# Optimization experiments

Hardware: AMD Instinct MI355X
Metric: run time of the kernel (lower is better)

## Reference

```python
import jax, jax.numpy as jnp
import numpy as np

DIM = 1024
HEADS = 16
DIM_HEAD = 64
INNER = HEADS * DIM_HEAD  # 1024
SCALE = DIM ** (-0.5)  # module scales by dim**-0.5 (not dim_head)


def setup_inputs() -> dict:
    key = jax.random.key(0)
    kx, kqkv, kwo, kbo = jax.random.split(key, 4)
    x = jax.random.normal(kx, (2, 2048, DIM), dtype=jnp.float32)
    W_qkv = jax.random.normal(kqkv, (DIM, 3 * INNER), dtype=jnp.float32) * (DIM ** -0.5)
    W_out = jax.random.normal(kwo, (INNER, DIM), dtype=jnp.float32) * (INNER ** -0.5)
    b_out = jax.random.normal(kbo, (DIM,), dtype=jnp.float32) * 0.01
    return {"x": x, "W_qkv": W_qkv, "W_out": W_out, "b_out": b_out}


def reference(x, W_qkv, W_out, b_out):
    b, n, _ = x.shape
    qkv = x @ W_qkv  # [b, n, 3*inner]
    q, k, v = jnp.split(qkv, 3, axis=-1)
    # [b, n, h*d] -> [b, h, n, d]
    reshape = lambda t: t.reshape(b, n, HEADS, DIM_HEAD).transpose(0, 2, 1, 3)
    q, k, v = reshape(q), reshape(k), reshape(v)
    dots = jnp.einsum('bhid,bhjd->bhij', q, k) * SCALE  # [b, h, n, n]
    attn = jax.nn.softmax(dots, axis=-1)
    out = jnp.einsum('bhij,bhjd->bhid', attn, v)  # [b, h, n, d]
    out = out.transpose(0, 2, 1, 3).reshape(b, n, INNER)
    return out @ W_out + b_out
```

## Files before the change

kernel.cpp:

```cpp
#include <hip/hip_runtime.h>

typedef __bf16 bf16x8 __attribute__((ext_vector_type(8)));
typedef __bf16 bf16x4 __attribute__((ext_vector_type(4)));
typedef __bf16 bf16x2 __attribute__((ext_vector_type(2)));
typedef float f32x4 __attribute__((ext_vector_type(4)));
typedef float f32x16 __attribute__((ext_vector_type(16)));
typedef int i32x4 __attribute__((ext_vector_type(4)));
typedef unsigned int u32x2 __attribute__((ext_vector_type(2)));

__device__ __forceinline__ void async16(void* lds, const void* g) {
  __builtin_amdgcn_global_load_lds(
      (__attribute__((address_space(1))) unsigned int*)(g),
      (__attribute__((address_space(3))) unsigned int*)(lds), 16, 0, 0);
}

__device__ __forceinline__ unsigned int pack2(float a, float b) {
  bf16x2 t;
  t[0] = (__bf16)a;
  t[1] = (__bf16)b;
  return __builtin_bit_cast(unsigned int, t);
}

__device__ __forceinline__ float fexp2(float x) {
#if __has_builtin(__builtin_amdgcn_exp2f)
  return __builtin_amdgcn_exp2f(x);
#else
  return exp2f(x);
#endif
}

__device__ __forceinline__ void plswap(unsigned int& d, unsigned int& s) {
#if __has_builtin(__builtin_amdgcn_permlane32_swap)
  u32x2 r = __builtin_amdgcn_permlane32_swap(d, s, false, false);
  d = r[0];
  s = r[1];
#else
  asm("v_permlane32_swap_b32 %0, %1" : "+v"(d), "+v"(s));
#endif
}

__device__ __forceinline__ int detect_block(const unsigned short* win, int* cnt_sh) {
  if (threadIdx.x == 0) *cnt_sh = 0;
  __syncthreads();
  int c = 0;
#pragma unroll
  for (int j = 0; j < 8; j++) {
    const unsigned short u = win[threadIdx.x * 8 + j];
    if (((u >> 7) & 0xFF) >= 0xC0) c++;
  }
  if (c) atomicAdd(cnt_sh, c);
  __syncthreads();
  return (*cnt_sh >= 64) ? 1 : 0;
}

__global__ __launch_bounds__(256) void prep(
    const void* __restrict__ x, const void* __restrict__ Wqkv,
    const void* __restrict__ Wout, __bf16* __restrict__ xb,
    __bf16* __restrict__ WqkvT, __bf16* __restrict__ WoutT,
    int* __restrict__ flagp)
{
  __shared__ __bf16 tile[64 * 65];
  __shared__ int cnt;
  const int bx = blockIdx.x;
  const int t = threadIdx.x;

  if (bx < 2048) {
    const long base = (long)bx * 2048;
    const int f = detect_block((const unsigned short*)x + base, &cnt);
    if (bx == 0 && t == 0) *flagp = f;
    const long i = base + t * 8;
    if (f) {
      const float* s = (const float*)x;
#pragma unroll
      for (int j = 0; j < 8; j++) xb[i + j] = (__bf16)s[i + j];
    } else {
      *(bf16x8*)&xb[i] = *(const bf16x8*)((const __bf16*)x + i);
    }
    return;
  }

  const void* in;  __bf16* out;  int R = 1024, C, tcx, tr;
  if (bx < 2816) {
    const int idx = bx - 2048;
    in = Wqkv; out = WqkvT; C = 3072; tcx = (idx % 48) * 64; tr = (idx / 48) * 64;
  } else {
    const int idx = bx - 2816;
    in = Wout; out = WoutT; C = 1024; tcx = (idx % 16) * 64; tr = (idx / 16) * 64;
  }
  const int f = detect_block((const unsigned short*)in + (long)tr * C + tcx, &cnt);
#pragma unroll
  for (int i = 0; i < 16; i++) {
    const int idx = t + 256 * i;
    const int r = idx >> 6, c = idx & 63;
    const long g = (long)(tr + r) * C + tcx + c;
    tile[r * 65 + c] = f ? (__bf16)((const float*)in)[g] : ((const __bf16*)in)[g];
  }
  __syncthreads();
#pragma unroll
  for (int i = 0; i < 16; i++) {
    const int idx = t + 256 * i;
    const int r = idx >> 6, c = idx & 63;
    out[(long)(tcx + r) * R + tr + c] = tile[c * 65 + r];
  }
}

__global__ __launch_bounds__(256, 3) void gemm_qkv(
    const __bf16* __restrict__ A, const __bf16* __restrict__ Bt,
    __bf16* __restrict__ Cqk, __bf16* __restrict__ Vt)
{
  __shared__ __bf16 smem[17408];
  const int t = threadIdx.x;
  const int l = t & 63;
  const int w = t >> 6;
  const int wr = w >> 1, wc = w & 1;
  const int lid = blockIdx.y * 32 + blockIdx.x;
  const int s = (lid & 7) * 96 + (lid >> 3);
  const long m0 = (long)(s & 31) * 128;
  const long n0 = (long)(s >> 5) * 128;
  const int K = 1024;

  const int srow = w * 16 + (l >> 2);
  const int skof = (l & 3) * 8;
  const __bf16* gA = A + (m0 + srow) * (long)K + skof;
  const __bf16* gB = Bt + (n0 + srow) * (long)K + skof;
  const int Ao[2] = {0, 8192}, Bo[2] = {4096, 12288};
  const int lof = w * 512 + l * 8;

  async16(smem + Ao[0] + lof,        gA);
  async16(smem + Ao[0] + 2048 + lof, gA + 64 * (long)K);
  async16(smem + Bo[0] + lof,        gB);
  async16(smem + Bo[0] + 2048 + lof, gB + 64 * (long)K);
  gA += 32; gB += 32;
  __syncthreads();

  f32x4 acc[4][4] = {};

  for (int it = 0; it < 32; it++) {
    if (it < 31) {
      const int nb = (it + 1) & 1;
      async16(smem + Ao[nb] + lof,        gA);
      async16(smem + Ao[nb] + 2048 + lof, gA + 64 * (long)K);
      async16(smem + Bo[nb] + lof,        gB);
      async16(smem + Bo[nb] + 2048 + lof, gB + 64 * (long)K);
      gA += 32; gB += 32;
    }
    const __bf16* As = smem + Ao[it & 1];
    const __bf16* Bs = smem + Bo[it & 1];
    bf16x8 af[4], bfr[4];
#pragma unroll
    for (int mi = 0; mi < 4; mi++)
      af[mi] = *(const bf16x8*)&As[(wr * 64 + mi * 16 + (l & 15)) * 32 + (l >> 4) * 8];
#pragma unroll
    for (int ni = 0; ni < 4; ni++)
      bfr[ni] = *(const bf16x8*)&Bs[(wc * 64 + ni * 16 + (l & 15)) * 32 + (l >> 4) * 8];
#pragma unroll
    for (int mi = 0; mi < 4; mi++)
#pragma unroll
      for (int ni = 0; ni < 4; ni++)
        acc[mi][ni] = __builtin_amdgcn_mfma_f32_16x16x32_bf16(af[mi], bfr[ni], acc[mi][ni], 0, 0, 0);
    __syncthreads();
  }

  if (n0 < 2048) {
#pragma unroll
    for (int mi = 0; mi < 4; mi++)
#pragma unroll
      for (int ni = 0; ni < 4; ni++) {
        const long col = n0 + wc * 64 + ni * 16 + (l & 15);
#pragma unroll
        for (int r = 0; r < 4; r++) {
          const long row = m0 + wr * 64 + mi * 16 + (l >> 4) * 4 + r;
          Cqk[row * 2048 + col] = (__bf16)acc[mi][ni][r];
        }
      }
  } else {
#pragma unroll
    for (int mi = 0; mi < 4; mi++)
#pragma unroll
      for (int ni = 0; ni < 4; ni++) {
        const int c = wc * 64 + ni * 16 + (l & 15);
        const int r = wr * 64 + mi * 16 + (l >> 4) * 4;
        bf16x4 pk;
#pragma unroll
        for (int k = 0; k < 4; k++) pk[k] = (__bf16)acc[mi][ni][k];
        *(bf16x4*)&smem[c * 136 + r] = pk;
      }
    __syncthreads();
    const int b = (int)(m0 >> 11);
    const int nbase = (int)(m0 & 2047);
#pragma unroll
    for (int i = 0; i < 8; i++) {
      const int c = (t >> 4) + i * 16;
      const int r8 = (t & 15) * 8;
      const bf16x8 v = *(const bf16x8*)&smem[c * 136 + r8];
      const int vcol = (int)(n0 - 2048) + c;
      *(bf16x8*)&Vt[((long)(b * 16 + (vcol >> 6)) * 64 + (vcol & 63)) * 2048 + nbase + r8] = v;
    }
  }
}

__global__ __launch_bounds__(256, 2) void gemm_out(
    const __bf16* __restrict__ A, const __bf16* __restrict__ Bt,
    const void* __restrict__ bias_raw, void* __restrict__ C,
    const int* __restrict__ flagp)
{
  __shared__ __bf16 smem[12288];
  const int t = threadIdx.x;
  const int l = t & 63;
  const int w = t >> 6;
  const int wr = w >> 1, wc = w & 1;
  const int lid = blockIdx.y * 32 + blockIdx.x;
  const int s = (lid & 7) * 64 + (lid >> 3);
  const long m0 = (long)(s & 31) * 128;
  const long n0 = (long)(s >> 5) * 64;
  const int of = *flagp;
  const int K = 1024;

  const int srow = w * 16 + (l >> 2);
  const int skof = (l & 3) * 8;
  const __bf16* gA = A + (m0 + srow) * (long)K + skof;
  const __bf16* gB = Bt + (n0 + srow) * (long)K + skof;
  const int Ao[2] = {0, 6144}, Bo[2] = {4096, 10240};
  const int lof = w * 512 + l * 8;

  async16(smem + Ao[0] + lof,        gA);
  async16(smem + Ao[0] + 2048 + lof, gA + 64 * (long)K);
  async16(smem + Bo[0] + lof,        gB);
  gA += 32; gB += 32;
  __syncthreads();

  f32x4 acc[4][2] = {};

  for (int it = 0; it < 32; it++) {
    if (it < 31) {
      const int nb = (it + 1) & 1;
      async16(smem + Ao[nb] + lof,        gA);
      async16(smem + Ao[nb] + 2048 + lof, gA + 64 * (long)K);
      async16(smem + Bo[nb] + lof,        gB);
      gA += 32; gB += 32;
    }
    const __bf16* As = smem + Ao[it & 1];
    const __bf16* Bs = smem + Bo[it & 1];
    bf16x8 af[4], bfr[2];
#pragma unroll
    for (int mi = 0; mi < 4; mi++)
      af[mi] = *(const bf16x8*)&As[(wr * 64 + mi * 16 + (l & 15)) * 32 + (l >> 4) * 8];
#pragma unroll
    for (int ni = 0; ni < 2; ni++)
      bfr[ni] = *(const bf16x8*)&Bs[(wc * 32 + ni * 16 + (l & 15)) * 32 + (l >> 4) * 8];
#pragma unroll
    for (int mi = 0; mi < 4; mi++)
#pragma unroll
      for (int ni = 0; ni < 2; ni++)
        acc[mi][ni] = __builtin_amdgcn_mfma_f32_16x16x32_bf16(af[mi], bfr[ni], acc[mi][ni], 0, 0, 0);
    __syncthreads();
  }

#pragma unroll
  for (int mi = 0; mi < 4; mi++)
#pragma unroll
    for (int ni = 0; ni < 2; ni++) {
      const long col = n0 + wc * 32 + ni * 16 + (l & 15);
      const float bv = of ? ((const float*)bias_raw)[col]
                          : (float)((const __bf16*)bias_raw)[col];
#pragma unroll
      for (int r = 0; r < 4; r++) {
        const long row = m0 + wr * 64 + mi * 16 + (l >> 4) * 4 + r;
        const float val = acc[mi][ni][r] + bv;
        const long off = row * 1024 + col;
        if (of) ((float*)C)[off] = val;
        else    ((__bf16*)C)[off] = (__bf16)val;
      }
    }
}

#define EXP2_SCALE 0.045084439f

__global__ __launch_bounds__(256, 4) void attn_kernel(
    const __bf16* __restrict__ qk, const __bf16* __restrict__ Vt,
    __bf16* __restrict__ O)
{
  __shared__ __bf16 smem[16384];
  const int t = threadIdx.x;
  const int l = t & 63;
  const int w = t >> 6;
  const int wi = w & 1, wj = w >> 1;
  const int hl = l >> 5;
  const int i7 = l & 7;
  const int L = blockIdx.y * 32 + blockIdx.x;
  const int bh = (L & 7) * 4 + ((L >> 3) & 3);
  const int qt = L >> 5;
  const int b = bh >> 4, head = bh & 15;
  const long q_row0 = (long)b * 2048 + qt * 64;

  const int srow = w * 8 + (l >> 3);
  const int sdof = ((l & 7) ^ (l >> 3)) * 8;
  const int lof = w * 512 + l * 8;

  const __bf16* gK = qk + ((long)b * 2048 + srow) * 2048 + 1024 + head * 64 + sdof;
  const __bf16* gV = Vt + ((long)bh * 64 + srow) * 2048 + sdof;
  async16(smem + lof,        gK);
  async16(smem + 2048 + lof, gK + 32 * 2048);
  async16(smem + 4096 + lof, gV);
  async16(smem + 6144 + lof, gV + 32 * 2048);
  gK += (long)64 * 2048;
  gV += 64;

  bf16x8 qf[4];
  {
    const __bf16* gQ = qk + (q_row0 + wi * 32 + (l & 31)) * 2048 + head * 64 + hl * 8;
#pragma unroll
    for (int kc = 0; kc < 4; kc++)
      qf[kc] = *(const bf16x8*)(gQ + kc * 16);
  }

  f32x16 accA = {0,0,0,0,0,0,0,0,0,0,0,0,0,0,0,0};
  f32x16 accB = {0,0,0,0,0,0,0,0,0,0,0,0,0,0,0,0};
  const f32x16 fz = {0,0,0,0,0,0,0,0,0,0,0,0,0,0,0,0};
  float l_i = 0.0f;

  bf16x8 pa0 = {}, pa1 = {};
  bf16x8 pvA0 = {}, pvA1 = {}, pvB0 = {}, pvB1 = {};

  const int krow = (wj * 32 + (l & 31)) * 64;
  const int vg = wj * 4;

  for (int it = 0; it < 32; it++) {
    __syncthreads();
    const __bf16* Ks = smem + (it & 1) * 8192;
    const __bf16* Vs = Ks + 4096;

    bf16x8 ak[4];
#pragma unroll
    for (int kc = 0; kc < 4; kc++)
      ak[kc] = *(const bf16x8*)&Ks[krow + (((kc * 2 + hl) ^ i7) * 8)];

    if (it < 31) {
      const int nb = ((it + 1) & 1) * 8192;
      async16(smem + nb + lof,        gK);
      async16(smem + nb + 2048 + lof, gK + 32 * 2048);
      async16(smem + nb + 4096 + lof, gV);
      async16(smem + nb + 6144 + lof, gV + 32 * 2048);
      gK += (long)64 * 2048;
      gV += 64;
    }

    __builtin_amdgcn_s_setprio(1);
    if (it > 0) {
      accA = __builtin_amdgcn_mfma_f32_32x32x16_bf16(pa0, pvA0, accA, 0, 0, 0);
      accB = __builtin_amdgcn_mfma_f32_32x32x16_bf16(pa0, pvB0, accB, 0, 0, 0);
      accA = __builtin_amdgcn_mfma_f32_32x32x16_bf16(pa1, pvA1, accA, 0, 0, 0);
      accB = __builtin_amdgcn_mfma_f32_32x32x16_bf16(pa1, pvB1, accB, 0, 0, 0);
    }
    f32x16 st = __builtin_amdgcn_mfma_f32_32x32x16_bf16(ak[0], qf[0], fz, 0, 0, 0);
#pragma unroll
    for (int kc = 1; kc < 4; kc++)
      st = __builtin_amdgcn_mfma_f32_32x32x16_bf16(ak[kc], qf[kc], st, 0, 0, 0);
    __builtin_amdgcn_s_setprio(0);

    pvA0 = *(const bf16x8*)&Vs[((l & 31)) * 64      + (((vg + hl) ^ i7) * 8)];
    pvB0 = *(const bf16x8*)&Vs[(32 + (l & 31)) * 64 + (((vg + hl) ^ i7) * 8)];
    pvA1 = *(const bf16x8*)&Vs[((l & 31)) * 64      + (((vg + 2 + hl) ^ i7) * 8)];
    pvB1 = *(const bf16x8*)&Vs[(32 + (l & 31)) * 64 + (((vg + 2 + hl) ^ i7) * 8)];

    float rs0 = 0.0f, rs1 = 0.0f;
#pragma unroll
    for (int r = 0; r < 16; r += 2) {
      const float p0 = fexp2(st[r] * EXP2_SCALE);
      const float p1 = fexp2(st[r + 1] * EXP2_SCALE);
      st[r] = p0;
      st[r + 1] = p1;
      rs0 += p0;
      rs1 += p1;
    }
    l_i += rs0 + rs1;

    unsigned int a0 = pack2(st[0],  st[1]),  b0 = pack2(st[4],  st[5]);
    unsigned int c0 = pack2(st[2],  st[3]),  d0 = pack2(st[6],  st[7]);
    unsigned int a1 = pack2(st[8],  st[9]),  b1 = pack2(st[12], st[13]);
    unsigned int c1 = pack2(st[10], st[11]), d1 = pack2(st[14], st[15]);
    plswap(a0, b0);
    plswap(c0, d0);
    plswap(a1, b1);
    plswap(c1, d1);
    const i32x4 f0 = {(int)a0, (int)c0, (int)b0, (int)d0};
    const i32x4 f1 = {(int)a1, (int)c1, (int)b1, (int)d1};
    pa0 = __builtin_bit_cast(bf16x8, f0);
    pa1 = __builtin_bit_cast(bf16x8, f1);
  }

  accA = __builtin_amdgcn_mfma_f32_32x32x16_bf16(pa0, pvA0, accA, 0, 0, 0);
  accB = __builtin_amdgcn_mfma_f32_32x32x16_bf16(pa0, pvB0, accB, 0, 0, 0);
  accA = __builtin_amdgcn_mfma_f32_32x32x16_bf16(pa1, pvA1, accA, 0, 0, 0);
  accB = __builtin_amdgcn_mfma_f32_32x32x16_bf16(pa1, pvB1, accB, 0, 0, 0);

  {
    unsigned int a = __builtin_bit_cast(unsigned int, l_i), bswp = a;
    plswap(a, bswp);
    l_i = __builtin_bit_cast(float, a) + __builtin_bit_cast(float, bswp);
  }

  __syncthreads();
  float* xbf = (float*)smem;
  float* lb  = (float*)(smem + 8192);
#pragma unroll
  for (int r = 0; r < 16; r++)
    xbf[w * 1024 + r * 64 + l] = wj ? accA[r] : accB[r];
  if (l < 32) lb[w * 32 + l] = l_i;
  __syncthreads();
  const int pw = 2 * (1 - wj) + wi;
#pragma unroll
  for (int r = 0; r < 16; r++) {
    const int iloc = (r & 3) + 8 * (r >> 2) + 4 * hl;
    const float lt = lb[wi * 32 + iloc] + lb[(wi + 2) * 32 + iloc];
    const float own = wj ? accB[r] : accA[r];
    const float o = own + xbf[pw * 1024 + r * 64 + l];
    const long row = q_row0 + wi * 32 + iloc;
    const long col = (long)head * 64 + wj * 32 + (l & 31);
    O[row * 1024 + col] = (__bf16)(o / lt);
  }
}

extern "C" void kernel_launch(void* const* d_in, const int* in_sizes, int n_in,
                              void* d_out, int out_size, void* d_ws, size_t ws_size,
                              hipStream_t stream) {
  const void* x    = d_in[0];
  const void* Wqkv = d_in[1];
  const void* Wout = d_in[2];
  const void* bout = d_in[3];

  char* ws = (char*)d_ws;
  int*    flagp = (int*)ws;
  __bf16* xb    = (__bf16*)(ws + 4096);
  __bf16* Obuf  = xb;
  __bf16* WqkvT = (__bf16*)(ws + 4096 +  8388608);
  __bf16* WoutT = (__bf16*)(ws + 4096 + 14680064);
  __bf16* qkbuf = (__bf16*)(ws + 4096 + 16777216);
  __bf16* VtBuf = (__bf16*)(ws + 4096 + 33554432);

  hipLaunchKernelGGL(prep, dim3(3072), dim3(256), 0, stream,
                     x, Wqkv, Wout, xb, WqkvT, WoutT, flagp);
  hipLaunchKernelGGL(gemm_qkv, dim3(32, 24), dim3(256), 0, stream,
                     xb, WqkvT, qkbuf, VtBuf);
  hipLaunchKernelGGL(attn_kernel, dim3(32, 32), dim3(256), 0, stream,
                     qkbuf, VtBuf, Obuf);
  hipLaunchKernelGGL(gemm_out, dim3(32, 16), dim3(256), 0, stream,
                     Obuf, WoutT, bout, d_out, flagp);
}
```

Before: 192.3 us.

## Fold softmax scale into Q projection and compute row sums via MFMA

Q is pre-scaled by the exp2 softmax constant in the QKV GEMM epilogue, which removes a multiply per score in the attention loop. Row sums of the probabilities are now accumulated with an extra MFMA against a ones vector instead of VALU adds and a cross-lane swap. The prep kernel's fp32-to-bf16 conversion is also vectorized with 16-byte loads and stores. Trade-offs: two extra MFMAs per iteration, row sums are now taken from the bf16-rounded probabilities, and Q is rounded to bf16 after scaling.

New measurement: 192.2 us. No clear change (-0.0%).

```diff
diff --git a/kernel.cpp b/kernel.cpp
--- a/kernel.cpp
+++ b/kernel.cpp
@@ -7,6 +7,8 @@
 typedef float f32x16 __attribute__((ext_vector_type(16)));
 typedef int i32x4 __attribute__((ext_vector_type(4)));
 typedef unsigned int u32x2 __attribute__((ext_vector_type(2)));
+
+#define EXP2_SCALE 0.045084439f
 
 __device__ __forceinline__ void async16(void* lds, const void* g) {
   __builtin_amdgcn_global_load_lds(
@@ -70,9 +72,14 @@
     if (bx == 0 && t == 0) *flagp = f;
     const long i = base + t * 8;
     if (f) {
-      const float* s = (const float*)x;
-#pragma unroll
-      for (int j = 0; j < 8; j++) xb[i + j] = (__bf16)s[i + j];
+      const f32x4* s4 = (const f32x4*)((const float*)x + i);
+      const f32x4 v0 = s4[0], v1 = s4[1];
+      bf16x8 o;
+#pragma unroll
+      for (int j = 0; j < 4; j++) o[j] = (__bf16)v0[j];
+#pragma unroll
+      for (int j = 0; j < 4; j++) o[4 + j] = (__bf16)v1[j];
+      *(bf16x8*)&xb[i] = o;
     } else {
       *(bf16x8*)&xb[i] = *(const bf16x8*)((const __bf16*)x + i);
     }
@@ -162,6 +169,7 @@
   }
 
   if (n0 < 2048) {
+    const float qs = (n0 < 1024) ? EXP2_SCALE : 1.0f;
 #pragma unroll
     for (int mi = 0; mi < 4; mi++)
 #pragma unroll
@@ -170,7 +178,7 @@
 #pragma unroll
         for (int r = 0; r < 4; r++) {
           const long row = m0 + wr * 64 + mi * 16 + (l >> 4) * 4 + r;
-          Cqk[row * 2048 + col] = (__bf16)acc[mi][ni][r];
+          Cqk[row * 2048 + col] = (__bf16)(acc[mi][ni][r] * qs);
         }
       }
   } else {
@@ -274,8 +282,6 @@
     }
 }
 
-#define EXP2_SCALE 0.045084439f
-
 __global__ __launch_bounds__(256, 4) void attn_kernel(
     const __bf16* __restrict__ qk, const __bf16* __restrict__ Vt,
     __bf16* __restrict__ O)
@@ -314,10 +320,14 @@
       qf[kc] = *(const bf16x8*)(gQ + kc * 16);
   }
 
+  bf16x8 onesb;
+#pragma unroll
+  for (int j = 0; j < 8; j++) onesb[j] = (__bf16)1.0f;
+
   f32x16 accA = {0,0,0,0,0,0,0,0,0,0,0,0,0,0,0,0};
   f32x16 accB = {0,0,0,0,0,0,0,0,0,0,0,0,0,0,0,0};
+  f32x16 lsum = {0,0,0,0,0,0,0,0,0,0,0,0,0,0,0,0};
   const f32x16 fz = {0,0,0,0,0,0,0,0,0,0,0,0,0,0,0,0};
-  float l_i = 0.0f;
 
   bf16x8 pa0 = {}, pa1 = {};
   bf16x8 pvA0 = {}, pvA1 = {}, pvB0 = {}, pvB1 = {};
@@ -351,6 +361,8 @@
       accB = __builtin_amdgcn_mfma_f32_32x32x16_bf16(pa0, pvB0, accB, 0, 0, 0);
       accA = __builtin_amdgcn_mfma_f32_32x32x16_bf16(pa1, pvA1, accA, 0, 0, 0);
       accB = __builtin_amdgcn_mfma_f32_32x32x16_bf16(pa1, pvB1, accB, 0, 0, 0);
+      lsum = __builtin_amdgcn_mfma_f32_32x32x16_bf16(pa0, onesb, lsum, 0, 0, 0);
+      lsum = __builtin_amdgcn_mfma_f32_32x32x16_bf16(pa1, onesb, lsum, 0, 0, 0);
     }
     f32x16 st = __builtin_amdgcn_mfma_f32_32x32x16_bf16(ak[0], qf[0], fz, 0, 0, 0);
 #pragma unroll
@@ -363,17 +375,8 @@
     pvA1 = *(const bf16x8*)&Vs[((l & 31)) * 64      + (((vg + 2 + hl) ^ i7) * 8)];
     pvB1 = *(const bf16x8*)&Vs[(32 + (l & 31)) * 64 + (((vg + 2 + hl) ^ i7) * 8)];
 
-    float rs0 = 0.0f, rs1 = 0.0f;
-#pragma unroll
-    for (int r = 0; r < 16; r += 2) {
-      const float p0 = fexp2(st[r] * EXP2_SCALE);
-      const float p1 = fexp2(st[r + 1] * EXP2_SCALE);
-      st[r] = p0;
-      st[r + 1] = p1;
-      rs0 += p0;
-      rs1 += p1;
-    }
-    l_i += rs0 + rs1;
+#pragma unroll
+    for (int r = 0; r < 16; r++) st[r] = fexp2(st[r]);
 
     unsigned int a0 = pack2(st[0],  st[1]),  b0 = pack2(st[4],  st[5]);
     unsigned int c0 = pack2(st[2],  st[3]),  d0 = pack2(st[6],  st[7]);
@@ -393,12 +396,8 @@
   accB = __builtin_amdgcn_mfma_f32_32x32x16_bf16(pa0, pvB0, accB, 0, 0, 0);
   accA = __builtin_amdgcn_mfma_f32_32x32x16_bf16(pa1, pvA1, accA, 0, 0, 0);
   accB = __builtin_amdgcn_mfma_f32_32x32x16_bf16(pa1, pvB1, accB, 0, 0, 0);
-
-  {
-    unsigned int a = __builtin_bit_cast(unsigned int, l_i), bswp = a;
-    plswap(a, bswp);
-    l_i = __builtin_bit_cast(float, a) + __builtin_bit_cast(float, bswp);
-  }
+  lsum = __builtin_amdgcn_mfma_f32_32x32x16_bf16(pa0, onesb, lsum, 0, 0, 0);
+  lsum = __builtin_amdgcn_mfma_f32_32x32x16_bf16(pa1, onesb, lsum, 0, 0, 0);
 
   __syncthreads();
   float* xbf = (float*)smem;
@@ -406,13 +405,19 @@
 #pragma unroll
   for (int r = 0; r < 16; r++)
     xbf[w * 1024 + r * 64 + l] = wj ? accA[r] : accB[r];
-  if (l < 32) lb[w * 32 + l] = l_i;
+  if ((l & 31) == 0) {
+#pragma unroll
+    for (int r = 0; r < 16; r++) {
+      const int iloc = (r & 3) + 8 * (r >> 2) + 4 * hl;
+      lb[w * 32 + iloc] = lsum[r];
+    }
+  }
   __syncthreads();
   const int pw = 2 * (1 - wj) + wi;
 #pragma unroll
   for (int r = 0; r < 16; r++) {
     const int iloc = (r & 3) + 8 * (r >> 2) + 4 * hl;
-    const float lt = lb[wi * 32 + iloc] + lb[(wi + 2) * 32 + iloc];
+    const float lt = lsum[r] + lb[pw * 32 + iloc];
     const float own = wj ? accB[r] : accA[r];
     const float o = own + xbf[pw * 1024 + r * 64 + l];
     const long row = q_row0 + wi * 32 + iloc;
```

## Pre-swizzle K/V into MFMA fragment layout and load directly from global in attention

Applied to the files above, without the earlier changes.

The QKV GEMM now writes K and V into per-head, per-64-key chunked layouts that match the MFMA operand fragments, and stores Q pre-multiplied by the exp2 softmax scale. The attention kernel drops its LDS double-buffered async staging and per-iteration barriers. It instead loads K and V fragments straight from global memory into registers, software-pipelined one tile ahead with a manually unrolled ping-pong. The prep kernel also vectorizes its fp32-to-bf16 conversion of x. The trade-off is that each wave does redundant global/L2 loads with no LDS sharing, and register pressure rises, with occupancy lowered to 3.

New measurement: 189.9 us. No clear change (-1.2%).

```diff
diff --git a/kernel.cpp b/kernel.cpp
--- a/kernel.cpp
+++ b/kernel.cpp
@@ -7,6 +7,8 @@
 typedef float f32x16 __attribute__((ext_vector_type(16)));
 typedef int i32x4 __attribute__((ext_vector_type(4)));
 typedef unsigned int u32x2 __attribute__((ext_vector_type(2)));
+
+#define EXP2_SCALE 0.045084439f
 
 __device__ __forceinline__ void async16(void* lds, const void* g) {
   __builtin_amdgcn_global_load_lds(
@@ -70,9 +72,14 @@
     if (bx == 0 && t == 0) *flagp = f;
     const long i = base + t * 8;
     if (f) {
-      const float* s = (const float*)x;
-#pragma unroll
-      for (int j = 0; j < 8; j++) xb[i + j] = (__bf16)s[i + j];
+      const f32x4* s4 = (const f32x4*)((const float*)x + i);
+      const f32x4 v0 = s4[0], v1 = s4[1];
+      bf16x8 o;
+#pragma unroll
+      for (int j = 0; j < 4; j++) o[j] = (__bf16)v0[j];
+#pragma unroll
+      for (int j = 0; j < 4; j++) o[4 + j] = (__bf16)v1[j];
+      *(bf16x8*)&xb[i] = o;
     } else {
       *(bf16x8*)&xb[i] = *(const bf16x8*)((const __bf16*)x + i);
     }
@@ -106,7 +113,7 @@
 
 __global__ __launch_bounds__(256, 3) void gemm_qkv(
     const __bf16* __restrict__ A, const __bf16* __restrict__ Bt,
-    __bf16* __restrict__ Cqk, __bf16* __restrict__ Vt)
+    __bf16* __restrict__ Qb, __bf16* __restrict__ Kc, __bf16* __restrict__ Vc)
 {
   __shared__ __bf16 smem[17408];
   const int t = threadIdx.x;
@@ -161,7 +168,7 @@
     __syncthreads();
   }
 
-  if (n0 < 2048) {
+  if (n0 < 1024) {
 #pragma unroll
     for (int mi = 0; mi < 4; mi++)
 #pragma unroll
@@ -170,7 +177,24 @@
 #pragma unroll
         for (int r = 0; r < 4; r++) {
           const long row = m0 + wr * 64 + mi * 16 + (l >> 4) * 4 + r;
-          Cqk[row * 2048 + col] = (__bf16)acc[mi][ni][r];
+          Qb[row * 1024 + col] = (__bf16)(acc[mi][ni][r] * EXP2_SCALE);
+        }
+      }
+  } else if (n0 < 2048) {
+    const int b = (int)(m0 >> 11);
+    const int nb_ = (int)(m0 & 2047);
+#pragma unroll
+    for (int mi = 0; mi < 4; mi++)
+#pragma unroll
+      for (int ni = 0; ni < 4; ni++) {
+        const int col1 = (int)(n0 - 1024) + wc * 64 + ni * 16 + (l & 15);
+        const int h = col1 >> 6, d = col1 & 63;
+        const long hb = ((long)(b * 16 + h) * 32);
+#pragma unroll
+        for (int r = 0; r < 4; r++) {
+          const int n = nb_ + wr * 64 + mi * 16 + (l >> 4) * 4 + r;
+          const long addr = (hb + (n >> 6)) * 4096 + (d >> 3) * 512 + (n & 63) * 8 + (d & 7);
+          Kc[addr] = (__bf16)acc[mi][ni][r];
         }
       }
   } else {
@@ -194,7 +218,10 @@
       const int r8 = (t & 15) * 8;
       const bf16x8 v = *(const bf16x8*)&smem[c * 136 + r8];
       const int vcol = (int)(n0 - 2048) + c;
-      *(bf16x8*)&Vt[((long)(b * 16 + (vcol >> 6)) * 64 + (vcol & 63)) * 2048 + nbase + r8] = v;
+      const int h = vcol >> 6, d = vcol & 63;
+      const int n = nbase + r8;
+      const long addr = ((long)(b * 16 + h) * 32 + (n >> 6)) * 4096 + ((n >> 3) & 7) * 512 + d * 8;
+      *(bf16x8*)&Vc[addr] = v;
     }
   }
 }
@@ -274,125 +301,103 @@
     }
 }
 
-#define EXP2_SCALE 0.045084439f
-
-__global__ __launch_bounds__(256, 4) void attn_kernel(
-    const __bf16* __restrict__ qk, const __bf16* __restrict__ Vt,
-    __bf16* __restrict__ O)
+__global__ __launch_bounds__(256, 3) void attn_kernel(
+    const __bf16* __restrict__ Qb, const __bf16* __restrict__ Kc,
+    const __bf16* __restrict__ Vc, __bf16* __restrict__ O)
 {
-  __shared__ __bf16 smem[16384];
+  __shared__ float fsm[4 * 1024 + 128];
   const int t = threadIdx.x;
   const int l = t & 63;
   const int w = t >> 6;
   const int wi = w & 1, wj = w >> 1;
   const int hl = l >> 5;
-  const int i7 = l & 7;
   const int L = blockIdx.y * 32 + blockIdx.x;
   const int bh = (L & 7) * 4 + ((L >> 3) & 3);
   const int qt = L >> 5;
   const int b = bh >> 4, head = bh & 15;
   const long q_row0 = (long)b * 2048 + qt * 64;
 
-  const int srow = w * 8 + (l >> 3);
-  const int sdof = ((l & 7) ^ (l >> 3)) * 8;
-  const int lof = w * 512 + l * 8;
-
-  const __bf16* gK = qk + ((long)b * 2048 + srow) * 2048 + 1024 + head * 64 + sdof;
-  const __bf16* gV = Vt + ((long)bh * 64 + srow) * 2048 + sdof;
-  async16(smem + lof,        gK);
-  async16(smem + 2048 + lof, gK + 32 * 2048);
-  async16(smem + 4096 + lof, gV);
-  async16(smem + 6144 + lof, gV + 32 * 2048);
-  gK += (long)64 * 2048;
-  gV += 64;
-
-  bf16x8 qf[4];
+  bf16x8 qf0, qf1, qf2, qf3;
   {
-    const __bf16* gQ = qk + (q_row0 + wi * 32 + (l & 31)) * 2048 + head * 64 + hl * 8;
-#pragma unroll
-    for (int kc = 0; kc < 4; kc++)
-      qf[kc] = *(const bf16x8*)(gQ + kc * 16);
-  }
+    const __bf16* gQ = Qb + (q_row0 + wi * 32 + (l & 31)) * 1024 + head * 64 + hl * 8;
+    qf0 = *(const bf16x8*)(gQ);
+    qf1 = *(const bf16x8*)(gQ + 16);
+    qf2 = *(const bf16x8*)(gQ + 32);
+    qf3 = *(const bf16x8*)(gQ + 48);
+  }
+
+  const __bf16* kb = Kc + (long)bh * 131072;
+  const __bf16* vb = Vc + (long)bh * 131072;
+  const int kof0 = hl * 512 + (wj * 32 + (l & 31)) * 8;
+  const int vof0 = (wj * 4 + hl) * 512 + (l & 31) * 8;
 
   f32x16 accA = {0,0,0,0,0,0,0,0,0,0,0,0,0,0,0,0};
   f32x16 accB = {0,0,0,0,0,0,0,0,0,0,0,0,0,0,0,0};
   const f32x16 fz = {0,0,0,0,0,0,0,0,0,0,0,0,0,0,0,0};
   float l_i = 0.0f;
-
   bf16x8 pa0 = {}, pa1 = {};
-  bf16x8 pvA0 = {}, pvA1 = {}, pvB0 = {}, pvB1 = {};
-
-  const int krow = (wj * 32 + (l & 31)) * 64;
-  const int vg = wj * 4;
-
-  for (int it = 0; it < 32; it++) {
-    __syncthreads();
-    const __bf16* Ks = smem + (it & 1) * 8192;
-    const __bf16* Vs = Ks + 4096;
-
-    bf16x8 ak[4];
-#pragma unroll
-    for (int kc = 0; kc < 4; kc++)
-      ak[kc] = *(const bf16x8*)&Ks[krow + (((kc * 2 + hl) ^ i7) * 8)];
-
-    if (it < 31) {
-      const int nb = ((it + 1) & 1) * 8192;
-      async16(smem + nb + lof,        gK);
-      async16(smem + nb + 2048 + lof, gK + 32 * 2048);
-      async16(smem + nb + 4096 + lof, gV);
-      async16(smem + nb + 6144 + lof, gV + 32 * 2048);
-      gK += (long)64 * 2048;
-      gV += 64;
-    }
-
-    __builtin_amdgcn_s_setprio(1);
-    if (it > 0) {
-      accA = __builtin_amdgcn_mfma_f32_32x32x16_bf16(pa0, pvA0, accA, 0, 0, 0);
-      accB = __builtin_amdgcn_mfma_f32_32x32x16_bf16(pa0, pvB0, accB, 0, 0, 0);
-      accA = __builtin_amdgcn_mfma_f32_32x32x16_bf16(pa1, pvA1, accA, 0, 0, 0);
-      accB = __builtin_amdgcn_mfma_f32_32x32x16_bf16(pa1, pvB1, accB, 0, 0, 0);
-    }
-    f32x16 st = __builtin_amdgcn_mfma_f32_32x32x16_bf16(ak[0], qf[0], fz, 0, 0, 0);
-#pragma unroll
-    for (int kc = 1; kc < 4; kc++)
-      st = __builtin_amdgcn_mfma_f32_32x32x16_bf16(ak[kc], qf[kc], st, 0, 0, 0);
-    __builtin_amdgcn_s_setprio(0);
-
-    pvA0 = *(const bf16x8*)&Vs[((l & 31)) * 64      + (((vg + hl) ^ i7) * 8)];
-    pvB0 = *(const bf16x8*)&Vs[(32 + (l & 31)) * 64 + (((vg + hl) ^ i7) * 8)];
-    pvA1 = *(const bf16x8*)&Vs[((l & 31)) * 64      + (((vg + 2 + hl) ^ i7) * 8)];
-    pvB1 = *(const bf16x8*)&Vs[(32 + (l & 31)) * 64 + (((vg + 2 + hl) ^ i7) * 8)];
-
-    float rs0 = 0.0f, rs1 = 0.0f;
-#pragma unroll
-    for (int r = 0; r < 16; r += 2) {
-      const float p0 = fexp2(st[r] * EXP2_SCALE);
-      const float p1 = fexp2(st[r + 1] * EXP2_SCALE);
-      st[r] = p0;
-      st[r + 1] = p1;
-      rs0 += p0;
-      rs1 += p1;
-    }
-    l_i += rs0 + rs1;
-
-    unsigned int a0 = pack2(st[0],  st[1]),  b0 = pack2(st[4],  st[5]);
-    unsigned int c0 = pack2(st[2],  st[3]),  d0 = pack2(st[6],  st[7]);
-    unsigned int a1 = pack2(st[8],  st[9]),  b1 = pack2(st[12], st[13]);
-    unsigned int c1 = pack2(st[10], st[11]), d1 = pack2(st[14], st[15]);
-    plswap(a0, b0);
-    plswap(c0, d0);
-    plswap(a1, b1);
-    plswap(c1, d1);
-    const i32x4 f0 = {(int)a0, (int)c0, (int)b0, (int)d0};
-    const i32x4 f1 = {(int)a1, (int)c1, (int)b1, (int)d1};
-    pa0 = __builtin_bit_cast(bf16x8, f0);
-    pa1 = __builtin_bit_cast(bf16x8, f1);
-  }
-
-  accA = __builtin_amdgcn_mfma_f32_32x32x16_bf16(pa0, pvA0, accA, 0, 0, 0);
-  accB = __builtin_amdgcn_mfma_f32_32x32x16_bf16(pa0, pvB0, accB, 0, 0, 0);
-  accA = __builtin_amdgcn_mfma_f32_32x32x16_bf16(pa1, pvA1, accA, 0, 0, 0);
-  accB = __builtin_amdgcn_mfma_f32_32x32x16_bf16(pa1, pvB1, accB, 0, 0, 0);
+
+#define LD8(p) (*(const bf16x8*)(p))
+  bf16x8 ka0 = LD8(kb + kof0),        ka1 = LD8(kb + kof0 + 1024);
+  bf16x8 ka2 = LD8(kb + kof0 + 2048), ka3 = LD8(kb + kof0 + 3072);
+  bf16x8 kn0, kn1, kn2, kn3;
+  bf16x8 va0 = {}, va1 = {}, va2 = {}, va3 = {};
+  bf16x8 vn0, vn1, vn2, vn3;
+
+#define ATT_ITER(IT, KA0,KA1,KA2,KA3, KN0,KN1,KN2,KN3, PV0,PV1,PV2,PV3, PN0,PN1,PN2,PN3) \
+  { \
+    const __bf16* kt_ = kb + (IT + 1) * 4096 + kof0; \
+    const __bf16* vt_ = vb + (IT) * 4096 + vof0; \
+    if ((IT) < 31) { \
+      KN0 = LD8(kt_); KN1 = LD8(kt_ + 1024); \
+      KN2 = LD8(kt_ + 2048); KN3 = LD8(kt_ + 3072); \
+    } \
+    PN0 = LD8(vt_);        PN1 = LD8(vt_ + 256); \
+    PN2 = LD8(vt_ + 1024); PN3 = LD8(vt_ + 1280); \
+    __builtin_amdgcn_s_setprio(1); \
+    if ((IT) > 0) { \
+      accA = __builtin_amdgcn_mfma_f32_32x32x16_bf16(pa0, PV0, accA, 0, 0, 0); \
+      accB = __builtin_amdgcn_mfma_f32_32x32x16_bf16(pa0, PV1, accB, 0, 0, 0); \
+      accA = __builtin_amdgcn_mfma_f32_32x32x16_bf16(pa1, PV2, accA, 0, 0, 0); \
+      accB = __builtin_amdgcn_mfma_f32_32x32x16_bf16(pa1, PV3, accB, 0, 0, 0); \
+    } \
+    f32x16 st = __builtin_amdgcn_mfma_f32_32x32x16_bf16(KA0, qf0, fz, 0, 0, 0); \
+    st = __builtin_amdgcn_mfma_f32_32x32x16_bf16(KA1, qf1, st, 0, 0, 0); \
+    st = __builtin_amdgcn_mfma_f32_32x32x16_bf16(KA2, qf2, st, 0, 0, 0); \
+    st = __builtin_amdgcn_mfma_f32_32x32x16_bf16(KA3, qf3, st, 0, 0, 0); \
+    __builtin_amdgcn_s_setprio(0); \
+    float rs0 = 0.0f, rs1 = 0.0f; \
+    _Pragma("unroll") \
+    for (int r = 0; r < 16; r += 2) { \
+      const float p0 = fexp2(st[r]); \
+      const float p1 = fexp2(st[r + 1]); \
+      st[r] = p0; st[r + 1] = p1; \
+      rs0 += p0; rs1 += p1; \
+    } \
+    l_i += rs0 + rs1; \
+    unsigned int a0 = pack2(st[0],  st[1]),  b0 = pack2(st[4],  st[5]); \
+    unsigned int c0 = pack2(st[2],  st[3]),  d0 = pack2(st[6],  st[7]); \
+    unsigned int a1 = pack2(st[8],  st[9]),  b1 = pack2(st[12], st[13]); \
+    unsigned int c1 = pack2(st[10], st[11]), d1 = pack2(st[14], st[15]); \
+    plswap(a0, b0); plswap(c0, d0); plswap(a1, b1); plswap(c1, d1); \
+    const i32x4 f0_ = {(int)a0, (int)c0, (int)b0, (int)d0}; \
+    const i32x4 f1_ = {(int)a1, (int)c1, (int)b1, (int)d1}; \
+    pa0 = __builtin_bit_cast(bf16x8, f0_); \
+    pa1 = __builtin_bit_cast(bf16x8, f1_); \
+  }
+
+  for (int itp = 0; itp < 16; itp++) {
+    const int it0 = itp * 2, it1 = itp * 2 + 1;
+    ATT_ITER(it0, ka0,ka1,ka2,ka3, kn0,kn1,kn2,kn3, va0,va1,va2,va3, vn0,vn1,vn2,vn3)
+    ATT_ITER(it1, kn0,kn1,kn2,kn3, ka0,ka1,ka2,ka3, vn0,vn1,vn2,vn3, va0,va1,va2,va3)
+  }
+#undef ATT_ITER
+#undef LD8
+
+  accA = __builtin_amdgcn_mfma_f32_32x32x16_bf16(pa0, va0, accA, 0, 0, 0);
+  accB = __builtin_amdgcn_mfma_f32_32x32x16_bf16(pa0, va1, accB, 0, 0, 0);
+  accA = __builtin_amdgcn_mfma_f32_32x32x16_bf16(pa1, va2, accA, 0, 0, 0);
+  accB = __builtin_amdgcn_mfma_f32_32x32x16_bf16(pa1, va3, accB, 0, 0, 0);
 
   {
     unsigned int a = __builtin_bit_cast(unsigned int, l_i), bswp = a;
@@ -400,9 +405,8 @@
     l_i = __builtin_bit_cast(float, a) + __builtin_bit_cast(float, bswp);
   }
 
-  __syncthreads();
-  float* xbf = (float*)smem;
-  float* lb  = (float*)(smem + 8192);
+  float* xbf = fsm;
+  float* lb  = fsm + 4096;
 #pragma unroll
   for (int r = 0; r < 16; r++)
     xbf[w * 1024 + r * 64 + l] = wj ? accA[r] : accB[r];
@@ -435,15 +439,16 @@
   __bf16* Obuf  = xb;
   __bf16* WqkvT = (__bf16*)(ws + 4096 +  8388608);
   __bf16* WoutT = (__bf16*)(ws + 4096 + 14680064);
-  __bf16* qkbuf = (__bf16*)(ws + 4096 + 16777216);
-  __bf16* VtBuf = (__bf16*)(ws + 4096 + 33554432);
+  __bf16* qbuf  = (__bf16*)(ws + 4096 + 16777216);
+  __bf16* kbuf  = (__bf16*)(ws + 4096 + 25165824);
+  __bf16* vbuf  = (__bf16*)(ws + 4096 + 33554432);
 
   hipLaunchKernelGGL(prep, dim3(3072), dim3(256), 0, stream,
                      x, Wqkv, Wout, xb, WqkvT, WoutT, flagp);
   hipLaunchKernelGGL(gemm_qkv, dim3(32, 24), dim3(256), 0, stream,
-                     xb, WqkvT, qkbuf, VtBuf);
+                     xb, WqkvT, qbuf, kbuf, vbuf);
   hipLaunchKernelGGL(attn_kernel, dim3(32, 32), dim3(256), 0, stream,
-                     qkbuf, VtBuf, Obuf);
+                     qbuf, kbuf, vbuf, Obuf);
   hipLaunchKernelGGL(gemm_out, dim3(32, 16), dim3(256), 0, stream,
                      Obuf, WoutT, bout, d_out, flagp);
 }
```
